# Kernel tuning notes

Hardware: AMD Instinct MI355X
Metric: run time of the kernel (lower is better)

## Reference

```python
import jax, jax.numpy as jnp
import numpy as np

EPS = 1e-12  # torch F.normalize eps


def setup_inputs() -> dict:
    key = jax.random.key(0)
    k1, k2 = jax.random.split(key)
    B, C, H, W = 8, 512, 96, 144
    M, D = 512, 512
    query_source = jax.random.normal(k1, (B, C, H, W), dtype=jnp.float32)
    mem = jax.random.uniform(k2, (M, D), dtype=jnp.float32)
    # Memory params are initialized as F.normalize(rand, dim=1)
    mem = mem / jnp.maximum(jnp.linalg.norm(mem, axis=1, keepdims=True), EPS)
    return {"query_source": query_source, "memory": mem}


def reference(query_source, memory):
    # forward(query_source, keys, only_update=False, query_target=None, fusion_keys=None)
    # -> self.read(normalize(query_source).permute(0,2,3,1), memory['3_0'])
    # L2-normalize over channel dim (dim=1), like F.normalize
    norm = jnp.linalg.norm(query_source, axis=1, keepdims=True)
    q = query_source / jnp.maximum(norm, EPS)
    q = jnp.transpose(q, (0, 2, 3, 1))  # [B, H, W, D]
    B, H, W, D = q.shape
    M = memory.shape[0]
    # get_score: score = query @ mem^T, then softmax over tokens (dim 0) and slots (dim 1)
    score = jnp.einsum('nd,md->nm', q.reshape(B * H * W, D), memory)  # [N, M]
    softmax_score_query = jax.nn.softmax(score, axis=0)
    softmax_score_memory = jax.nn.softmax(score, axis=1)
    # read: updated_query = score_memory.detach() @ memory
    updated_query = jax.lax.stop_gradient(softmax_score_memory) @ memory  # [N, D]
    updated_query = updated_query.reshape(B, H, W, D).transpose(0, 3, 1, 2)  # [B, D, H, W]
    return updated_query, softmax_score_query, softmax_score_memory
```

## Files before the change

### kernel.cpp

```cpp
#include <hip/hip_runtime.h>
#include <hip/hip_bf16.h>
#include <cstdint>
#include <cstddef>

#define HWIMG 13824
#define NTOK  110592
#define CDIM  512

typedef float  floatx4  __attribute__((ext_vector_type(4)));
typedef __bf16 bf16x8   __attribute__((ext_vector_type(8)));
typedef unsigned short ushortx8 __attribute__((ext_vector_type(8)));

__device__ __forceinline__ unsigned short f2bf(float f) {
  unsigned int u = __float_as_uint(f);
  u += 0x7FFFu + ((u >> 16) & 1u);
  return (unsigned short)(u >> 16);
}
__device__ __forceinline__ float bf2f(unsigned short u) {
  return __uint_as_float(((unsigned int)u) << 16);
}

#define GLL16(g, l)                                                                \
  __builtin_amdgcn_global_load_lds((const __attribute__((address_space(1))) void*)(g), \
                                   (__attribute__((address_space(3))) void*)(l), 16, 0, 0)

__global__ __launch_bounds__(256) void convert_mem_kernel(
    const float* __restrict__ mem, unsigned short* __restrict__ membf,
    unsigned short* __restrict__ memTbf) {
  int g = blockIdx.x * 256 + threadIdx.x;
  int m = g >> 9, d = g & 511;
  unsigned short b = f2bf(mem[g]);
  membf[g] = b;
  memTbf[d * 512 + m] = b;
}

__global__ __launch_bounds__(256) void normalize_kernel(
    const float* __restrict__ qs, unsigned short* __restrict__ qbf) {
  __shared__ float red[4][64];
  __shared__ float inv[64];
  __shared__ float tile[64][65];
  const int t = threadIdx.x;
  const int n0 = blockIdx.x * 64;
  const int b = n0 / HWIMG;
  const int r0 = n0 % HWIMG;
  const float* base = qs + (size_t)b * 512 * HWIMG + r0;
  const int tok = t & 63, cp = t >> 6;

  float ssq = 0.f;
  for (int c = cp; c < 512; c += 4) {
    float x = base[(size_t)c * HWIMG + tok];
    ssq += x * x;
  }
  red[cp][tok] = ssq;
  __syncthreads();
  if (t < 64) {
    float s = red[0][t] + red[1][t] + red[2][t] + red[3][t];
    inv[t] = 1.0f / fmaxf(sqrtf(s), 1e-12f);
  }
  __syncthreads();

  for (int cc = 0; cc < 8; cc++) {
#pragma unroll
    for (int i = 0; i < 16; i++) {
      int cl = (t >> 6) + i * 4;
      tile[cl][tok] = base[(size_t)(cc * 64 + cl) * HWIMG + tok];
    }
    __syncthreads();
    const int c_out = t & 63;
    const int tg = t >> 6;
#pragma unroll
    for (int i = 0; i < 16; i++) {
      int tk = tg * 16 + i;
      float v = tile[c_out][tk] * inv[tk];
      qbf[(size_t)(n0 + tk) * 512 + cc * 64 + c_out] = f2bf(v);
    }
    __syncthreads();
  }
}

#define GEMM_DECLS                                                         \
  __shared__ unsigned short lds[32768];       \
  const int t = threadIdx.x;                                               \
  const int lane = t & 63, wid = t >> 6;                                   \
  const int quad = lane >> 4, li = lane & 15;                              \
  const int n0 = blockIdx.x * 128;                                         \
  const int am = (wid & 1) * 4, bn = (wid >> 1) * 4;                       \
  const int wm = (wid & 1) * 64, wn = (wid >> 1) * 64;                     \
  const int row0 = ((t >> 7) << 4) | (t & 15);                             \
  const int koff = ((t >> 6) & 1) * 64 + ((t >> 4) & 3) * 16;              \
  char* ldsb = (char*)lds;

#define STAGE(buf, sidx) do {                                              \
    const char* a_ = gA + (((sidx) & 7) << 7);                             \
    const char* b_ = gB0 + (((sidx) >> 3) * 131072) + (((sidx) & 7) << 7); \
    char* la_ = ldsb + (buf) * 32768 + t * 16;                             \
    char* lb_ = la_ + 16384;                                               \
    GLL16(a_, la_);          GLL16(a_ + 32768, la_ + 4096);                \
    GLL16(a_ + 65536, la_ + 8192); GLL16(a_ + 98304, la_ + 12288);         \
    GLL16(b_, lb_);          GLL16(b_ + 32768, lb_ + 4096);                \
    GLL16(b_ + 65536, lb_ + 8192); GLL16(b_ + 98304, lb_ + 12288);         \
  } while (0)

#define COMPUTE(buf) do {                                                  \
    const unsigned short* Ac = lds + (buf) * 16384;                        \
    const unsigned short* Bc = Ac + 8192;                                  \
    _Pragma("unroll")                                                      \
    for (int h = 0; h < 2; h++) {                                          \
      bf16x8 af[4], bfv[4];                                                \
      _Pragma("unroll")                                                    \
      for (int i = 0; i < 4; i++)                                          \
        af[i] = *(const bf16x8*)&Ac[((((am + i) * 2 + h) << 6) | lane) * 8]; \
      _Pragma("unroll")                                                    \
      for (int j = 0; j < 4; j++)                                          \
        bfv[j] = *(const bf16x8*)&Bc[((((bn + j) * 2 + h) << 6) | lane) * 8]; \
      _Pragma("unroll")                                                    \
      for (int i = 0; i < 4; i++)                                          \
        _Pragma("unroll")                                                  \
        for (int j = 0; j < 4; j++)                                        \
          acc[i][j] = __builtin_amdgcn_mfma_f32_16x16x32_bf16(             \
              af[i], bfv[j], acc[i][j], 0, 0, 0);                          \
    }                                                                      \
  } while (0)

#define ACC_ZERO do {                                                     \
    floatx4 z_ = {0.f, 0.f, 0.f, 0.f};                                    \
    _Pragma("unroll")                                                     \
    for (int i = 0; i < 4; i++)                                           \
      _Pragma("unroll")                                                   \
      for (int j = 0; j < 4; j++) acc[i][j] = z_;                         \
  } while (0)

#define VMCNT0 asm volatile("s_waitcnt vmcnt(0)" ::: "memory")

__global__ __launch_bounds__(256, 2) void gemm1_kernel(
    const unsigned short* __restrict__ A, const unsigned short* __restrict__ Bm,
    unsigned short* __restrict__ Ebf, float* __restrict__ colsum,
    float* __restrict__ rowsum) {
  GEMM_DECLS
  __shared__ float cs_lds[512];
  __shared__ float rs_lds[128];
  cs_lds[t] = 0.f; cs_lds[t + 256] = 0.f;
  if (t < 128) rs_lds[t] = 0.f;
  const char* gA = (const char*)A + (size_t)(n0 + row0) * 1024 + koff;
  const char* gB0 = (const char*)Bm + (size_t)row0 * 1024 + koff;
  float racc[4][4];
#pragma unroll
  for (int i = 0; i < 4; i++)
#pragma unroll
    for (int r = 0; r < 4; r++) racc[i][r] = 0.f;
  floatx4 acc[4][4];
  ACC_ZERO;

  STAGE(0, 0);
  VMCNT0;
  __syncthreads();
#pragma unroll 1
  for (int s = 0; s < 32; ++s) {
    const int cur = s & 1;
    if (s < 31) STAGE(cur ^ 1, s + 1);
    COMPUTE(cur);
    VMCNT0;
    __syncthreads();
    if ((s & 7) == 7) {
      const int mt = s >> 3;
      float cp[4] = {0.f, 0.f, 0.f, 0.f};
#pragma unroll
      for (int i = 0; i < 4; i++) {
#pragma unroll
        for (int r = 0; r < 4; r++) {
          const int row = n0 + wm + i * 16 + quad * 4 + r;
          float rowacc = 0.f;
#pragma unroll
          for (int j = 0; j < 4; j++) {
            float e = __expf(acc[i][j][r]);
            const int col = mt * 128 + wn + j * 16 + li;
            Ebf[(size_t)row * 512 + col] = f2bf(e);
            cp[j] += e;
            rowacc += e;
          }
          racc[i][r] += rowacc;
        }
      }
#pragma unroll
      for (int j = 0; j < 4; j++) {
        float c = cp[j];
        c += __shfl_xor(c, 16, 64);
        c += __shfl_xor(c, 32, 64);
        if (lane < 16) atomicAdd(&cs_lds[mt * 128 + wn + j * 16 + li], c);
      }
      ACC_ZERO;
    }
  }

#pragma unroll
  for (int i = 0; i < 4; i++) {
#pragma unroll
    for (int r = 0; r < 4; r++) {
      float v = racc[i][r];
      v += __shfl_xor(v, 1, 64);
      v += __shfl_xor(v, 2, 64);
      v += __shfl_xor(v, 4, 64);
      v += __shfl_xor(v, 8, 64);
      if (li == 0) atomicAdd(&rs_lds[wm + i * 16 + quad * 4 + r], v);
    }
  }
  __syncthreads();
  if (t < 128) rowsum[n0 + t] = rs_lds[t];
  atomicAdd(&colsum[t], cs_lds[t]);
  atomicAdd(&colsum[t + 256], cs_lds[t + 256]);
}

__global__ __launch_bounds__(256, 2) void gemm2_kernel(
    const unsigned short* __restrict__ P, const unsigned short* __restrict__ BmT,
    const float* __restrict__ rowsum, const float* __restrict__ colsum,
    float* __restrict__ out0, float* __restrict__ out1, float* __restrict__ out2) {
  GEMM_DECLS
  __shared__ __align__(16) float inv_cs[512];
  __shared__ __align__(16) float inv_rs[128];
  inv_cs[t] = 1.0f / colsum[t];
  inv_cs[t + 256] = 1.0f / colsum[t + 256];
  if (t < 128) inv_rs[t] = 1.0f / rowsum[n0 + t];
  const char* gA = (const char*)P + (size_t)(n0 + row0) * 1024 + koff;
  const char* gB0 = (const char*)BmT + (size_t)row0 * 1024 + koff;
  const int bimg = n0 / HWIMG;
  const int r0 = n0 % HWIMG;
  floatx4 acc[4][4];
  ACC_ZERO;

  STAGE(0, 0);
  VMCNT0;
  __syncthreads();
#pragma unroll 1
  for (int s = 0; s < 32; ++s) {
    const int cur = s & 1;
    if (s < 31) STAGE(cur ^ 1, s + 1);
    COMPUTE(cur);
    VMCNT0;
    __syncthreads();
    if (s < 8) {
      const int cbase = s * 64 + (koff >> 1);
      const floatx4 rca = *(const floatx4*)&inv_cs[cbase];
      const floatx4 rcb = *(const floatx4*)&inv_cs[cbase + 4];
#pragma unroll
      for (int sh = 0; sh < 4; ++sh) {
        ushortx8 ev = *(const ushortx8*)(ldsb + cur * 32768 + t * 16 + sh * 4096);
        const float rr = inv_rs[row0 + 32 * sh];
        floatx4 e0, e1;
        e0[0] = bf2f(ev[0]); e0[1] = bf2f(ev[1]); e0[2] = bf2f(ev[2]); e0[3] = bf2f(ev[3]);
        e1[0] = bf2f(ev[4]); e1[1] = bf2f(ev[5]); e1[2] = bf2f(ev[6]); e1[3] = bf2f(ev[7]);
        const size_t off = (size_t)(n0 + row0 + 32 * sh) * 512 + cbase;
        *(floatx4*)&out1[off]     = e0 * rca;
        *(floatx4*)&out1[off + 4] = e1 * rcb;
        *(floatx4*)&out2[off]     = e0 * rr;
        *(floatx4*)&out2[off + 4] = e1 * rr;
      }
    }
    if ((s & 7) == 7) {
      const int mt = s >> 3;
#pragma unroll
      for (int i = 0; i < 4; i++) {
        const int rb = r0 + wm + i * 16 + quad * 4;
        const floatx4 riv = *(const floatx4*)&inv_rs[wm + i * 16 + quad * 4];
#pragma unroll
        for (int j = 0; j < 4; j++) {
          const int col = mt * 128 + wn + j * 16 + li;
          *(floatx4*)&out0[(size_t)(bimg * 512 + col) * HWIMG + rb] =
              acc[i][j] * riv;
        }
      }
      ACC_ZERO;
    }
  }
}

extern "C" void kernel_launch(void* const* d_in, const int* in_sizes, int n_in,
                              void* d_out, int out_size, void* d_ws, size_t ws_size,
                              hipStream_t stream) {
  const float* qs  = (const float*)d_in[0];
  const float* mem = (const float*)d_in[1];

  float* out0 = (float*)d_out;
  float* out1 = out0 + (size_t)NTOK * 512;
  float* out2 = out1 + (size_t)NTOK * 512;

  char* ws = (char*)d_ws;
  unsigned short* qbf    = (unsigned short*)ws;
  unsigned short* Ebf    = (unsigned short*)(ws + 113246208);
  unsigned short* membf  = (unsigned short*)(ws + 226492416);
  unsigned short* memTbf = (unsigned short*)(ws + 227016704);
  float* colsum          = (float*)(ws + 227540992);
  float* rowsum          = (float*)(ws + 227543040);

  hipMemsetAsync(colsum, 0, 2048, stream);
  convert_mem_kernel<<<1024, 256, 0, stream>>>(mem, membf, memTbf);
  normalize_kernel<<<NTOK / 64, 256, 0, stream>>>(qs, qbf);
  gemm1_kernel<<<NTOK / 128, 256, 0, stream>>>(qbf, membf, Ebf, colsum, rowsum);
  gemm2_kernel<<<NTOK / 128, 256, 0, stream>>>(Ebf, memTbf, rowsum, colsum,
                                               out0, out1, out2);
}
```

Before: 1.211 ms.

## Defer GEMM epilogue stores and use partial vmcnt waits to overlap with MFMA

```diff
diff --git a/kernel.cpp b/kernel.cpp
--- a/kernel.cpp
+++ b/kernel.cpp
@@ -130,7 +130,36 @@
       for (int j = 0; j < 4; j++) acc[i][j] = z_;                         \
   } while (0)
 
-#define VMCNT0 asm volatile("s_waitcnt vmcnt(0)" ::: "memory")
+#define WAITV(n) asm volatile("s_waitcnt vmcnt(" #n ")" ::: "memory")
+
+#define G1_EPILOGUE(mt)                                                    \
+  do {                                                                     \
+    float cp[4] = {0.f, 0.f, 0.f, 0.f};                                    \
+    _Pragma("unroll")                                                      \
+    for (int i = 0; i < 4; i++) {                                          \
+      _Pragma("unroll")                                                    \
+      for (int r = 0; r < 4; r++) {                                        \
+        const int row = n0 + wm + i * 16 + quad * 4 + r;                   \
+        float rowacc = 0.f;                                                \
+        _Pragma("unroll")                                                  \
+        for (int j = 0; j < 4; j++) {                                      \
+          float e = __expf(acc[i][j][r]);   \
+          const int col = (mt) * 128 + wn + j * 16 + li;                   \
+          Ebf[(size_t)row * 512 + col] = f2bf(e);                          \
+          cp[j] += e;                                                      \
+          rowacc += e;                                                     \
+        }                                                                  \
+        racc[i][r] += rowacc;                                              \
+      }                                                                    \
+    }                                                                      \
+    _Pragma("unroll")                                                      \
+    for (int j = 0; j < 4; j++) {                                          \
+      float c = cp[j];                                                     \
+      c += __shfl_xor(c, 16, 64);                                          \
+      c += __shfl_xor(c, 32, 64);                                          \
+      if (lane < 16) atomicAdd(&cs_lds[(mt) * 128 + wn + j * 16 + li], c); \
+    }                                                                      \
+  } while (0)
 
 __global__ __launch_bounds__(256, 2) void gemm1_kernel(
     const unsigned short* __restrict__ A, const unsigned short* __restrict__ Bm,
@@ -152,45 +181,25 @@
   ACC_ZERO;
 
   STAGE(0, 0);
-  VMCNT0;
+  WAITV(0);
   __syncthreads();
 #pragma unroll 1
   for (int s = 0; s < 32; ++s) {
     const int cur = s & 1;
     if (s < 31) STAGE(cur ^ 1, s + 1);
+    if (s && (s & 7) == 0) {
+      G1_EPILOGUE((s >> 3) - 1);
+      ACC_ZERO;
+    }
     COMPUTE(cur);
-    VMCNT0;
+    if (s == 8 || s == 16 || s == 24) {
+      WAITV(48);
+    } else {
+      WAITV(0);
+    }
     __syncthreads();
-    if ((s & 7) == 7) {
-      const int mt = s >> 3;
-      float cp[4] = {0.f, 0.f, 0.f, 0.f};
-#pragma unroll
-      for (int i = 0; i < 4; i++) {
-#pragma unroll
-        for (int r = 0; r < 4; r++) {
-          const int row = n0 + wm + i * 16 + quad * 4 + r;
-          float rowacc = 0.f;
-#pragma unroll
-          for (int j = 0; j < 4; j++) {
-            float e = __expf(acc[i][j][r]);
-            const int col = mt * 128 + wn + j * 16 + li;
-            Ebf[(size_t)row * 512 + col] = f2bf(e);
-            cp[j] += e;
-            rowacc += e;
-          }
-          racc[i][r] += rowacc;
-        }
-      }
-#pragma unroll
-      for (int j = 0; j < 4; j++) {
-        float c = cp[j];
-        c += __shfl_xor(c, 16, 64);
-        c += __shfl_xor(c, 32, 64);
-        if (lane < 16) atomicAdd(&cs_lds[mt * 128 + wn + j * 16 + li], c);
-      }
-      ACC_ZERO;
-    }
-  }
+  }
+  G1_EPILOGUE(3);
 
 #pragma unroll
   for (int i = 0; i < 4; i++) {
@@ -209,6 +218,21 @@
   atomicAdd(&colsum[t], cs_lds[t]);
   atomicAdd(&colsum[t + 256], cs_lds[t + 256]);
 }
+
+#define G2_OUT0(mt)                                                        \
+  do {                                                                     \
+    _Pragma("unroll")                                                      \
+    for (int i = 0; i < 4; i++) {                                          \
+      const int rb = r0 + wm + i * 16 + quad * 4;                          \
+      const floatx4 riv = *(const floatx4*)&inv_rs[wm + i * 16 + quad * 4];\
+      _Pragma("unroll")                                                    \
+      for (int j = 0; j < 4; j++) {                                        \
+        const int col = (mt) * 128 + wn + j * 16 + li;            \
+        *(floatx4*)&out0[(size_t)(bimg * 512 + col) * HWIMG + rb] =        \
+            acc[i][j] * riv;                                               \
+      }                                                                    \
+    }                                                                      \
+  } while (0)
 
 __global__ __launch_bounds__(256, 2) void gemm2_kernel(
     const unsigned short* __restrict__ P, const unsigned short* __restrict__ BmT,
@@ -226,28 +250,28 @@
   const int r0 = n0 % HWIMG;
   floatx4 acc[4][4];
   ACC_ZERO;
+  ushortx8 ev[4];
 
   STAGE(0, 0);
-  VMCNT0;
+  WAITV(0);
   __syncthreads();
 #pragma unroll 1
   for (int s = 0; s < 32; ++s) {
     const int cur = s & 1;
     if (s < 31) STAGE(cur ^ 1, s + 1);
-    COMPUTE(cur);
-    VMCNT0;
-    __syncthreads();
-    if (s < 8) {
-      const int cbase = s * 64 + (koff >> 1);
+    if (s >= 1 && s <= 8) {
+      const int sp = s - 1;
+      const int cbase = sp * 64 + (koff >> 1);
       const floatx4 rca = *(const floatx4*)&inv_cs[cbase];
       const floatx4 rcb = *(const floatx4*)&inv_cs[cbase + 4];
 #pragma unroll
       for (int sh = 0; sh < 4; ++sh) {
-        ushortx8 ev = *(const ushortx8*)(ldsb + cur * 32768 + t * 16 + sh * 4096);
         const float rr = inv_rs[row0 + 32 * sh];
         floatx4 e0, e1;
-        e0[0] = bf2f(ev[0]); e0[1] = bf2f(ev[1]); e0[2] = bf2f(ev[2]); e0[3] = bf2f(ev[3]);
-        e1[0] = bf2f(ev[4]); e1[1] = bf2f(ev[5]); e1[2] = bf2f(ev[6]); e1[3] = bf2f(ev[7]);
+        e0[0] = bf2f(ev[sh][0]); e0[1] = bf2f(ev[sh][1]);
+        e0[2] = bf2f(ev[sh][2]); e0[3] = bf2f(ev[sh][3]);
+        e1[0] = bf2f(ev[sh][4]); e1[1] = bf2f(ev[sh][5]);
+        e1[2] = bf2f(ev[sh][6]); e1[3] = bf2f(ev[sh][7]);
         const size_t off = (size_t)(n0 + row0 + 32 * sh) * 512 + cbase;
         *(floatx4*)&out1[off]     = e0 * rca;
         *(floatx4*)&out1[off + 4] = e1 * rcb;
@@ -255,22 +279,28 @@
         *(floatx4*)&out2[off + 4] = e1 * rr;
       }
     }
-    if ((s & 7) == 7) {
-      const int mt = s >> 3;
-#pragma unroll
-      for (int i = 0; i < 4; i++) {
-        const int rb = r0 + wm + i * 16 + quad * 4;
-        const floatx4 riv = *(const floatx4*)&inv_rs[wm + i * 16 + quad * 4];
-#pragma unroll
-        for (int j = 0; j < 4; j++) {
-          const int col = mt * 128 + wn + j * 16 + li;
-          *(floatx4*)&out0[(size_t)(bimg * 512 + col) * HWIMG + rb] =
-              acc[i][j] * riv;
-        }
-      }
+    if (s && (s & 7) == 0) {
+      G2_OUT0((s >> 3) - 1);
       ACC_ZERO;
     }
-  }
+    if (s < 8) {
+#pragma unroll
+      for (int sh = 0; sh < 4; ++sh)
+        ev[sh] = *(const ushortx8*)(ldsb + cur * 32768 + t * 16 + sh * 4096);
+    }
+    COMPUTE(cur);
+    if (s >= 1 && s <= 7) {
+      WAITV(16);
+    } else if (s == 8) {
+      WAITV(32);
+    } else if (s == 16 || s == 24) {
+      WAITV(16);
+    } else {
+      WAITV(0);
+    }
+    __syncthreads();
+  }
+  G2_OUT0(3);
 }
 
 extern "C" void kernel_launch(void* const* d_in, const int* in_sizes, int n_in,
```

Result: no change. 1.215 ms (+0.3%).
